# Kernel optimization log

Measured on AMD Instinct MI355X. Metric: run time of the kernel, lower is better.

Reference implementation:

```python
import jax, jax.numpy as jnp
import numpy as np

B, S, D, H, BS = 4, 4096, 1024, 16, 256
DH = D // H  # 64
NB = S // BS  # 16 blocks


def setup_inputs() -> dict:
    key = jax.random.key(0)
    ks = jax.random.split(key, 16)
    sc = 1.0 / np.sqrt(D).astype(np.float32)

    def lin(k):
        return jax.random.normal(k, (D, D), jnp.float32) * sc

    zb = jnp.zeros((D,), jnp.float32)
    return {
        "x": jax.random.normal(ks[0], (B, S, D), jnp.float32),
        "lq_w": lin(ks[1]), "lq_b": zb,
        "lk_w": lin(ks[2]), "lk_b": zb,
        "lv_w": lin(ks[3]), "lv_b": zb,
        "lo_w": lin(ks[4]), "lo_b": zb,
        "pos_bias": jax.random.normal(ks[5], (1, H, BS, BS), jnp.float32) * 0.1,
        "sq_w": lin(ks[6]), "sq_b": zb,
        "sk_w": lin(ks[7]), "sk_b": zb,
        "sv_w": lin(ks[8]), "sv_b": zb,
        "so_w": lin(ks[9]), "so_b": zb,
        "sum_w": lin(ks[10]), "sum_b": zb,
    }


def _mha(x, qw, qb, kw, kb, vw, vb, ow, ob, bias=None):
    # x: [N, L, D] -> multi-head attention, optional additive position bias.
    N, L, _ = x.shape
    q = (x @ qw + qb).reshape(N, L, H, DH).transpose(0, 2, 1, 3)  # [N,H,L,DH]
    k = (x @ kw + kb).reshape(N, L, H, DH).transpose(0, 2, 1, 3)
    v = (x @ vw + vb).reshape(N, L, H, DH).transpose(0, 2, 1, 3)
    scores = jnp.einsum("nhqd,nhkd->nhqk", q, k) / jnp.sqrt(jnp.float32(DH))
    if bias is not None:
        scores = scores + bias[:, :, :L, :L]
    w = jax.nn.softmax(scores, axis=-1)
    ctx = jnp.einsum("nhqk,nhkd->nhqd", w, v)
    ctx = ctx.transpose(0, 2, 1, 3).reshape(N, L, D)
    return ctx @ ow + ob


def reference(x, lq_w, lq_b, lk_w, lk_b, lv_w, lv_b, lo_w, lo_b, pos_bias,
              sq_w, sq_b, sk_w, sk_b, sv_w, sv_b, so_w, so_b, sum_w, sum_b):
    # Local block attention with learned position bias (seq already multiple of BS)
    xb = x.reshape(B * NB, BS, D)
    local = _mha(xb, lq_w, lq_b, lk_w, lk_b, lv_w, lv_b, lo_w, lo_b,
                 bias=pos_bias).reshape(B, S, D)
    # Block summaries: mean-pool each block then linear summarizer
    summaries = x.reshape(B, NB, BS, D).mean(axis=2) @ sum_w + sum_b  # [B,NB,D]
    # Global attention over block summaries (no position bias)
    summ = _mha(summaries, sq_w, sq_b, sk_w, sk_b, sv_w, sv_b, so_w, so_b)
    # Broadcast each block's summary context back to its tokens and combine
    summ_exp = jnp.repeat(summ, BS, axis=1)  # [B,S,D]
    return local + summ_exp
```

## Files before the change

### kernel.cpp

```cpp
#include <hip/hip_runtime.h>
#include <hip/hip_bf16.h>

typedef unsigned short u16;
typedef __bf16 bf16x8 __attribute__((ext_vector_type(8)));
typedef float floatx4 __attribute__((ext_vector_type(4)));
typedef unsigned short u16x4 __attribute__((ext_vector_type(4)));
typedef unsigned short u16x8 __attribute__((ext_vector_type(8)));

__device__ __forceinline__ float b2f(u16 v) {
  unsigned u = ((unsigned)v) << 16;
  return __builtin_bit_cast(float, u);
}
__device__ __forceinline__ u16 f2b(float f) {
  unsigned u = __builtin_bit_cast(unsigned, f);
  unsigned r = (u + 0x7FFFu + ((u >> 16) & 1u)) >> 16;
  return (u16)r;
}
__device__ __forceinline__ void cp16(const u16* g, u16* l) {
  __builtin_amdgcn_global_load_lds(
      (const __attribute__((address_space(1))) unsigned int*)g,
      (__attribute__((address_space(3))) unsigned int*)l, 16, 0, 0);
}

struct GemmArgs {
  const u16* A;
  const u16* BT0; const u16* BT1; const u16* BT2;
  const float* b0; const float* b1; const float* b2;
  const float* summ;
  int srow0;
  u16* C0; u16* C1; u16* C2;
  float* Cf;
};

__global__ __launch_bounds__(256, 2) void gemm_bt(GemmArgs g) {
  const int z = blockIdx.z;
  const u16* A      = g.A;
  const u16* BT     = (z == 0) ? g.BT0 : (z == 1 ? g.BT1 : g.BT2);
  const float* bias = (z == 0) ? g.b0  : (z == 1 ? g.b1  : g.b2);
  u16* C            = (z == 0) ? g.C0  : (z == 1 ? g.C1  : g.C2);

  __shared__ u16 As[128 * 32];
  __shared__ u16 Bs[128 * 32];

  const int tid  = threadIdx.x;
  const int lane = tid & 63;
  const int wave = tid >> 6;
  const int quad = lane >> 4;
  const int cl   = lane & 15;
  const int wm   = wave & 1;
  const int wn   = wave >> 1;

  const size_t row0 = (size_t)blockIdx.x * 128;
  const size_t col0 = (size_t)blockIdx.y * 128;

  const int srow = lane >> 2;
  const int soff = (lane & 3) << 3;

  const u16* gA0 = A + (row0 + (size_t)(wave * 16 + srow)) * 1024 + soff;
  const u16* gA1 = gA0 + (size_t)64 * 1024;
  const u16* gB0 = BT + (col0 + (size_t)(wave * 16 + srow)) * 1024 + soff;
  const u16* gB1 = gB0 + (size_t)64 * 1024;
  u16* lA0 = As + wave * 512 + lane * 8;
  u16* lA1 = lA0 + 2048;
  u16* lB0 = Bs + wave * 512 + lane * 8;
  u16* lB1 = lB0 + 2048;

  floatx4 acc[4][4] = {};

  for (int kt = 0; kt < 1024; kt += 32) {
    __syncthreads();
    cp16(gA0, lA0); cp16(gA1, lA1);
    cp16(gB0, lB0); cp16(gB1, lB1);
    gA0 += 32; gA1 += 32; gB0 += 32; gB1 += 32;
    __syncthreads();
    bf16x8 af[4], bfr[4];
#pragma unroll
    for (int m = 0; m < 4; ++m)
      af[m] = *(const bf16x8*)&As[(wm * 64 + m * 16 + cl) * 32 + quad * 8];
#pragma unroll
    for (int n = 0; n < 4; ++n)
      bfr[n] = *(const bf16x8*)&Bs[(wn * 64 + n * 16 + cl) * 32 + quad * 8];
#pragma unroll
    for (int m = 0; m < 4; ++m)
#pragma unroll
      for (int n = 0; n < 4; ++n)
        acc[m][n] = __builtin_amdgcn_mfma_f32_16x16x32_bf16(af[m], bfr[n],
                                                            acc[m][n], 0, 0, 0);
  }

  const float* summ = g.summ;
#pragma unroll
  for (int m = 0; m < 4; ++m) {
    const size_t rbase = row0 + wm * 64 + m * 16 + quad * 4;
#pragma unroll
    for (int n = 0; n < 4; ++n) {
      const size_t c = col0 + wn * 64 + n * 16 + cl;
      const float bb = bias[c];
#pragma unroll
      for (int e = 0; e < 4; ++e) {
        float v = acc[m][n][e] + bb;
        if (summ)
          v += summ[(size_t)((int)((rbase + e) >> 8) + g.srow0) * 1024 + c];
        if (g.Cf) g.Cf[(rbase + e) * 1024 + c] = v;
        else      C[(rbase + e) * 1024 + c] = f2b(v);
      }
    }
  }
}

__global__ __launch_bounds__(256, 2) void local_attn(
    const u16* __restrict__ Q, const u16* __restrict__ Kt,
    const u16* __restrict__ Vt, const float* __restrict__ pbias,
    u16* __restrict__ ctx) {
  const int qt  = blockIdx.x;
  const int h   = blockIdx.y;
  const int blk = blockIdx.z;
  const int tid  = threadIdx.x;
  const int lane = tid & 63;
  const int w    = tid >> 6;
  const int quad = lane >> 4;
  const int cl   = lane & 15;

  __shared__ u16 BufA[64 * 72];
  __shared__ u16 BufB[64 * 72];

  const size_t tok0  = (size_t)blk * 256;
  const size_t qrow0 = tok0 + qt * 64;
  const int hc = h * 64;

  for (int i = tid; i < 512; i += 256) {
    const int row = i >> 3, c8 = (i & 7) * 8;
    *(u16x8*)&BufA[row * 72 + c8] =
        *(const u16x8*)&Q[(qrow0 + row) * 1024 + hc + c8];
  }

  floatx4 accS[16] = {};
#pragma unroll
  for (int kc = 0; kc < 4; ++kc) {
    __syncthreads();
    for (int i = tid; i < 512; i += 256) {
      const int row = i >> 3, c8 = (i & 7) * 8;
      *(u16x8*)&BufB[row * 72 + c8] =
          *(const u16x8*)&Kt[(tok0 + kc * 64 + row) * 1024 + hc + c8];
    }
    __syncthreads();
#pragma unroll
    for (int ki = 0; ki < 2; ++ki) {
      const bf16x8 aq =
          *(const bf16x8*)&BufA[(w * 16 + cl) * 72 + ki * 32 + quad * 8];
#pragma unroll
      for (int n = 0; n < 4; ++n) {
        const bf16x8 bk =
            *(const bf16x8*)&BufB[(n * 16 + cl) * 72 + ki * 32 + quad * 8];
        accS[kc * 4 + n] = __builtin_amdgcn_mfma_f32_16x16x32_bf16(
            aq, bk, accS[kc * 4 + n], 0, 0, 0);
      }
    }
  }

  float mrow[4] = {-1e30f, -1e30f, -1e30f, -1e30f};
#pragma unroll
  for (int r = 0; r < 4; ++r) {
    const float* brow = pbias + ((size_t)h << 16) +
                        (size_t)(qt * 64 + w * 16 + quad * 4 + r) * 256 + cl;
#pragma unroll
    for (int n = 0; n < 16; ++n) {
      float s = accS[n][r] * 0.125f + brow[n * 16];
      accS[n][r] = s;
      mrow[r] = fmaxf(mrow[r], s);
    }
  }
#pragma unroll
  for (int r = 0; r < 4; ++r) {
#pragma unroll
    for (int st = 1; st < 16; st <<= 1)
      mrow[r] = fmaxf(mrow[r], __shfl_xor(mrow[r], st));
  }
  float lsum[4] = {0.f, 0.f, 0.f, 0.f};
#pragma unroll
  for (int n = 0; n < 16; ++n) {
#pragma unroll
    for (int r = 0; r < 4; ++r) {
      float p = exp2f((accS[n][r] - mrow[r]) * 1.44269504f);
      accS[n][r] = p;
      lsum[r] += p;
    }
  }
#pragma unroll
  for (int r = 0; r < 4; ++r) {
#pragma unroll
    for (int st = 1; st < 16; st <<= 1)
      lsum[r] += __shfl_xor(lsum[r], st);
  }

  floatx4 accO[4] = {};
#pragma unroll
  for (int kc = 0; kc < 4; ++kc) {
    __syncthreads();
#pragma unroll
    for (int nn = 0; nn < 4; ++nn)
#pragma unroll
      for (int r = 0; r < 4; ++r)
        BufA[(w * 16 + quad * 4 + r) * 72 + nn * 16 + cl] =
            f2b(accS[kc * 4 + nn][r]);
    for (int i = tid; i < 512; i += 256) {
      const int key = i & 63, dh0 = (i >> 6) * 8;
      u16x8 v = *(const u16x8*)&Vt[(tok0 + kc * 64 + key) * 1024 + hc + dh0];
#pragma unroll
      for (int j = 0; j < 8; ++j) BufB[(dh0 + j) * 72 + key] = v[j];
    }
    __syncthreads();
#pragma unroll
    for (int ki = 0; ki < 2; ++ki) {
      const bf16x8 ap =
          *(const bf16x8*)&BufA[(w * 16 + cl) * 72 + ki * 32 + quad * 8];
#pragma unroll
      for (int nd = 0; nd < 4; ++nd) {
        const bf16x8 bv =
            *(const bf16x8*)&BufB[(nd * 16 + cl) * 72 + ki * 32 + quad * 8];
        accO[nd] = __builtin_amdgcn_mfma_f32_16x16x32_bf16(ap, bv, accO[nd],
                                                           0, 0, 0);
      }
    }
  }

  float inv[4];
#pragma unroll
  for (int r = 0; r < 4; ++r) inv[r] = 1.0f / lsum[r];
#pragma unroll
  for (int nd = 0; nd < 4; ++nd)
#pragma unroll
    for (int r = 0; r < 4; ++r)
      ctx[(qrow0 + w * 16 + quad * 4 + r) * 1024 + hc + nd * 16 + cl] =
          f2b(accO[nd][r] * inv[r]);
}

__global__ void cvt_x(const float* __restrict__ x, u16* __restrict__ xb) {
  const size_t i = ((size_t)blockIdx.x * 256 + threadIdx.x) * 4;
  float4 v = *(const float4*)&x[i];
  u16x4 o;
  o[0] = f2b(v.x); o[1] = f2b(v.y); o[2] = f2b(v.z); o[3] = f2b(v.w);
  *(u16x4*)&xb[i] = o;
}

__global__ void block_mean(const float* __restrict__ x, u16* __restrict__ xm) {
  const int g = blockIdx.x >> 2;
  const int d = ((blockIdx.x & 3) << 8) + threadIdx.x;
  const float* p = x + (size_t)g * 256 * 1024 + d;
  float s = 0.f;
  for (int t = 0; t < 256; ++t) s += p[(size_t)t * 1024];
  xm[(size_t)g * 1024 + d] = f2b(s * (1.0f / 256.0f));
}

__global__ void summ_attn(const u16* __restrict__ SQ, const u16* __restrict__ SK,
                          const u16* __restrict__ SV, u16* __restrict__ sctx) {
  const int b = blockIdx.x >> 4;
  const int h = blockIdx.x & 15;
  const int t = threadIdx.x;
  __shared__ float Qf[16][64];
  __shared__ float Kf[16][64];
  __shared__ float Vf[16][64];
  __shared__ float sc[16][16];
  for (int i = t; i < 1024; i += 64) {
    const int r = i >> 6, d = i & 63;
    const size_t off = (size_t)(b * 16 + r) * 1024 + h * 64 + d;
    Qf[r][d] = b2f(SQ[off]);
    Kf[r][d] = b2f(SK[off]);
    Vf[r][d] = b2f(SV[off]);
  }
  __syncthreads();
  {
    const int i = t >> 2, j0 = t & 3;
#pragma unroll
    for (int jj = 0; jj < 4; ++jj) {
      const int j = j0 + jj * 4;
      float s = 0.f;
      for (int d = 0; d < 64; ++d) s += Qf[i][d] * Kf[j][d];
      sc[i][j] = s * 0.125f;
    }
  }
  __syncthreads();
  if (t < 16) {
    float m = -1e30f;
    for (int j = 0; j < 16; ++j) m = fmaxf(m, sc[t][j]);
    float l = 0.f;
    for (int j = 0; j < 16; ++j) {
      float p = exp2f((sc[t][j] - m) * 1.44269504f);
      sc[t][j] = p;
      l += p;
    }
    const float inv = 1.0f / l;
    for (int j = 0; j < 16; ++j) sc[t][j] *= inv;
  }
  __syncthreads();
  {
    const int i = t >> 2, d0 = (t & 3) * 16;
    for (int dd = 0; dd < 16; ++dd) {
      float a = 0.f;
      for (int j = 0; j < 16; ++j) a += sc[i][j] * Vf[j][d0 + dd];
      sctx[(size_t)(b * 16 + i) * 1024 + h * 64 + d0 + dd] = f2b(a);
    }
  }
}

struct TPtrs { const float* src[9]; u16* dst[9]; };

__global__ void cvt_transpose9(TPtrs p) {
  const float* src = p.src[blockIdx.z];
  u16* dst         = p.dst[blockIdx.z];
  __shared__ u16 tile[64][72];
  const int r0 = blockIdx.x * 64, c0 = blockIdx.y * 64;
  for (int i = threadIdx.x; i < 1024; i += 256) {
    const int row = i >> 4, c4 = (i & 15) * 4;
    float4 v = *(const float4*)&src[(size_t)(r0 + row) * 1024 + c0 + c4];
    tile[row][c4 + 0] = f2b(v.x);
    tile[row][c4 + 1] = f2b(v.y);
    tile[row][c4 + 2] = f2b(v.z);
    tile[row][c4 + 3] = f2b(v.w);
  }
  __syncthreads();
  for (int i = threadIdx.x; i < 512; i += 256) {
    const int row = i >> 3, c8 = (i & 7) * 8;
    u16x8 v;
#pragma unroll
    for (int j = 0; j < 8; ++j) v[j] = tile[c8 + j][row];
    *(u16x8*)&dst[(size_t)(c0 + row) * 1024 + r0 + c8] = v;
  }
}

extern "C" void kernel_launch(void* const* d_in, const int* in_sizes, int n_in,
                              void* d_out, int out_size, void* d_ws, size_t ws_size,
                              hipStream_t stream) {
  const float* x    = (const float*)d_in[0];
  const float* lqw  = (const float*)d_in[1];
  const float* lqb  = (const float*)d_in[2];
  const float* lkw  = (const float*)d_in[3];
  const float* lkb  = (const float*)d_in[4];
  const float* lvw  = (const float*)d_in[5];
  const float* lvb  = (const float*)d_in[6];
  const float* low_ = (const float*)d_in[7];
  const float* lob  = (const float*)d_in[8];
  const float* pb   = (const float*)d_in[9];
  const float* sqw  = (const float*)d_in[10];
  const float* sqb  = (const float*)d_in[11];
  const float* skw  = (const float*)d_in[12];
  const float* skb  = (const float*)d_in[13];
  const float* svw  = (const float*)d_in[14];
  const float* svb  = (const float*)d_in[15];
  const float* sow  = (const float*)d_in[16];
  const float* sob  = (const float*)d_in[17];
  const float* smw  = (const float*)d_in[18];
  const float* smb  = (const float*)d_in[19];

  char* W = (char*)d_ws;
  size_t off = 0;
  u16* wt[9];
  for (int i = 0; i < 9; ++i) { wt[i] = (u16*)(W + off); off += (size_t)1024 * 1024 * 2; }
  u16* Xb  = (u16*)(W + off); off += (size_t)16384 * 1024 * 2;
  u16* XM  = (u16*)(W + off); off += (size_t)128 * 1024 * 2;
  u16* SMR = (u16*)(W + off); off += (size_t)128 * 1024 * 2;
  u16* SQp = (u16*)(W + off); off += (size_t)128 * 1024 * 2;
  u16* SKp = (u16*)(W + off); off += (size_t)128 * 1024 * 2;
  u16* SVp = (u16*)(W + off); off += (size_t)128 * 1024 * 2;
  u16* SCT = (u16*)(W + off); off += (size_t)128 * 1024 * 2;
  float* SMM = (float*)(W + off); off += (size_t)128 * 1024 * 4;
  const size_t fixedB = off;

  int CH = 256;
  for (int c = 16384; c >= 256; c >>= 1) {
    if (fixedB + (size_t)4 * c * 1024 * 2 <= ws_size) { CH = c; break; }
  }
  u16* Qb  = (u16*)(W + fixedB);
  u16* Kb  = Qb + (size_t)CH * 1024;
  u16* Vb  = Kb + (size_t)CH * 1024;
  u16* CTX = Vb + (size_t)CH * 1024;

  TPtrs tp;
  tp.src[0] = lqw; tp.src[1] = lkw; tp.src[2] = lvw; tp.src[3] = low_;
  tp.src[4] = sqw; tp.src[5] = skw; tp.src[6] = svw; tp.src[7] = sow;
  tp.src[8] = smw;
  for (int i = 0; i < 9; ++i) tp.dst[i] = wt[i];
  cvt_transpose9<<<dim3(16, 16, 9), 256, 0, stream>>>(tp);

  cvt_x<<<dim3(16384), 256, 0, stream>>>(x, Xb);
  block_mean<<<dim3(256), 256, 0, stream>>>(x, XM);

  GemmArgs g1{};
  g1.A = XM; g1.BT0 = g1.BT1 = g1.BT2 = wt[8];
  g1.b0 = g1.b1 = g1.b2 = smb; g1.summ = nullptr; g1.srow0 = 0;
  g1.C0 = g1.C1 = g1.C2 = SMR; g1.Cf = nullptr;
  gemm_bt<<<dim3(1, 8, 1), 256, 0, stream>>>(g1);

  GemmArgs g2{};
  g2.A = SMR; g2.BT0 = wt[4]; g2.BT1 = wt[5]; g2.BT2 = wt[6];
  g2.b0 = sqb; g2.b1 = skb; g2.b2 = svb; g2.summ = nullptr; g2.srow0 = 0;
  g2.C0 = SQp; g2.C1 = SKp; g2.C2 = SVp; g2.Cf = nullptr;
  gemm_bt<<<dim3(1, 8, 3), 256, 0, stream>>>(g2);

  summ_attn<<<dim3(64), 64, 0, stream>>>(SQp, SKp, SVp, SCT);

  GemmArgs g3{};
  g3.A = SCT; g3.BT0 = g3.BT1 = g3.BT2 = wt[7];
  g3.b0 = g3.b1 = g3.b2 = sob; g3.summ = nullptr; g3.srow0 = 0;
  g3.C0 = g3.C1 = g3.C2 = nullptr; g3.Cf = SMM;
  gemm_bt<<<dim3(1, 8, 1), 256, 0, stream>>>(g3);

  for (int base = 0; base < 16384; base += CH) {
    GemmArgs g4{};
    g4.A = Xb + (size_t)base * 1024;
    g4.BT0 = wt[0]; g4.BT1 = wt[1]; g4.BT2 = wt[2];
    g4.b0 = lqb; g4.b1 = lkb; g4.b2 = lvb; g4.summ = nullptr; g4.srow0 = 0;
    g4.C0 = Qb; g4.C1 = Kb; g4.C2 = Vb; g4.Cf = nullptr;
    gemm_bt<<<dim3(CH / 128, 8, 3), 256, 0, stream>>>(g4);

    local_attn<<<dim3(4, 16, CH / 256), 256, 0, stream>>>(Qb, Kb, Vb, pb, CTX);

    GemmArgs g5{};
    g5.A = CTX; g5.BT0 = g5.BT1 = g5.BT2 = wt[3];
    g5.b0 = g5.b1 = g5.b2 = lob; g5.summ = SMM; g5.srow0 = base >> 8;
    g5.C0 = g5.C1 = g5.C2 = nullptr;
    g5.Cf = (float*)d_out + (size_t)base * 1024;
    gemm_bt<<<dim3(CH / 128, 8, 1), 256, 0, stream>>>(g5);
  }

  (void)in_sizes; (void)n_in; (void)out_size;
}
```

Measured before the change: 531.4 us.

## Add 256x256-tile 8-wave GEMM with double-buffered async LDS pipeline

```diff
diff --git a/kernel.cpp b/kernel.cpp
--- a/kernel.cpp
+++ b/kernel.cpp
@@ -92,6 +92,155 @@
 #pragma unroll
   for (int m = 0; m < 4; ++m) {
     const size_t rbase = row0 + wm * 64 + m * 16 + quad * 4;
+#pragma unroll
+    for (int n = 0; n < 4; ++n) {
+      const size_t c = col0 + wn * 64 + n * 16 + cl;
+      const float bb = bias[c];
+#pragma unroll
+      for (int e = 0; e < 4; ++e) {
+        float v = acc[m][n][e] + bb;
+        if (summ)
+          v += summ[(size_t)((int)((rbase + e) >> 8) + g.srow0) * 1024 + c];
+        if (g.Cf) g.Cf[(rbase + e) * 1024 + c] = v;
+        else      C[(rbase + e) * 1024 + c] = f2b(v);
+      }
+    }
+  }
+}
+
+__global__ __launch_bounds__(512, 2) void gemm_bt256(GemmArgs g) {
+  extern __shared__ char lds[];
+  const int z = blockIdx.z;
+  const u16* A      = g.A;
+  const u16* BT     = (z == 0) ? g.BT0 : (z == 1 ? g.BT1 : g.BT2);
+  const float* bias = (z == 0) ? g.b0  : (z == 1 ? g.b1  : g.b2);
+  u16* C            = (z == 0) ? g.C0  : (z == 1 ? g.C1  : g.C2);
+
+  const int tid  = threadIdx.x;
+  const int lane = tid & 63;
+  const int w    = tid >> 6;
+  const int q    = lane >> 4;
+  const int cl   = lane & 15;
+  const int wm   = w >> 2;
+  const int wn   = w & 3;
+
+  const size_t row0 = (size_t)blockIdx.x * 256;
+  const size_t col0 = (size_t)blockIdx.y * 256;
+
+  const int lr  = lane >> 3;
+  const int lcs = ((lane & 7) ^ lr) * 8;
+  const u16* Ab = A  + (row0 + (size_t)lr) * 1024 + lcs;
+  const u16* Bb = BT + (col0 + (size_t)lr) * 1024 + lcs;
+  const int wa8 = w * 8;
+  const int wbr = (w >> 2) * 64 + (w & 3) * 8;
+
+  const int swz  = (cl & 7) << 4;
+  const int aRd0 = (wm * 128 + cl) * 128 + ((q * 16) ^ swz);
+  const int aRd1 = aRd0 ^ 64;
+  const int bRd0 = 32768 + (wn * 64 + cl) * 128 + ((q * 16) ^ swz);
+  const int bRd1 = bRd0 ^ 64;
+
+  floatx4 acc[8][4] = {};
+
+#define STAGE_A(QA, T, BUF)                                                   \
+  {                                                                           \
+    const int r0s = (QA) * 64 + wa8;                                          \
+    cp16(Ab + (size_t)r0s * 1024 + (T) * 64,                                  \
+         (u16*)(lds + (BUF) * 65536 + r0s * 128));                            \
+    const int r1s = r0s + 128;                                                \
+    cp16(Ab + (size_t)r1s * 1024 + (T) * 64,                                  \
+         (u16*)(lds + (BUF) * 65536 + r1s * 128));                            \
+  }
+
+#define STAGE_B(QB, T, BUF)                                                   \
+  {                                                                           \
+    const int r0s = wbr + (QB) * 32;                                          \
+    cp16(Bb + (size_t)r0s * 1024 + (T) * 64,                                  \
+         (u16*)(lds + (BUF) * 65536 + 32768 + r0s * 128));                    \
+    const int r1s = r0s + 128;                                                \
+    cp16(Bb + (size_t)r1s * 1024 + (T) * 64,                                  \
+         (u16*)(lds + (BUF) * 65536 + 32768 + r1s * 128));                    \
+  }
+
+#define PHASE(BUF, QM, QN, STAGE, WAIT)                                       \
+  {                                                                           \
+    char* Lb = lds + (BUF) * 65536;                                           \
+    bf16x8 aF0[4], aF1[4], bF0[2], bF1[2];                                    \
+    _Pragma("unroll")                                                         \
+    for (int mm = 0; mm < 4; ++mm) {                                          \
+      const int ro = ((QM) * 64 + mm * 16) * 128;                             \
+      aF0[mm] = *(const bf16x8*)(Lb + (aRd0 + ro));                           \
+      aF1[mm] = *(const bf16x8*)(Lb + (aRd1 + ro));                           \
+    }                                                                         \
+    _Pragma("unroll")                                                         \
+    for (int nn = 0; nn < 2; ++nn) {                                          \
+      const int co = ((QN) * 32 + nn * 16) * 128;                             \
+      bF0[nn] = *(const bf16x8*)(Lb + (bRd0 + co));                           \
+      bF1[nn] = *(const bf16x8*)(Lb + (bRd1 + co));                           \
+    }                                                                         \
+    STAGE                                                                     \
+    asm volatile("s_barrier" ::: "memory");                                   \
+    asm volatile("s_waitcnt lgkmcnt(0)" ::: "memory");                        \
+    __builtin_amdgcn_s_setprio(1);                                            \
+    _Pragma("unroll")                                                         \
+    for (int mm = 0; mm < 4; ++mm)                                            \
+      _Pragma("unroll")                                                       \
+      for (int nn = 0; nn < 2; ++nn)                                          \
+        acc[(QM) * 4 + mm][(QN) * 2 + nn] =                                   \
+            __builtin_amdgcn_mfma_f32_16x16x32_bf16(                          \
+                aF0[mm], bF0[nn], acc[(QM) * 4 + mm][(QN) * 2 + nn], 0, 0, 0);\
+    _Pragma("unroll")                                                         \
+    for (int mm = 0; mm < 4; ++mm)                                            \
+      _Pragma("unroll")                                                       \
+      for (int nn = 0; nn < 2; ++nn)                                          \
+        acc[(QM) * 4 + mm][(QN) * 2 + nn] =                                   \
+            __builtin_amdgcn_mfma_f32_16x16x32_bf16(                          \
+                aF1[mm], bF1[nn], acc[(QM) * 4 + mm][(QN) * 2 + nn], 0, 0, 0);\
+    __builtin_amdgcn_s_setprio(0);                                            \
+    WAIT                                                                      \
+    asm volatile("s_barrier" ::: "memory");                                   \
+  }
+
+#define TILE_MAIN(BUF, U)                                                     \
+  PHASE(BUF, 0, 0, { STAGE_A(1, (U) + 1, (BUF) ^ 1); }, {})                   \
+  PHASE(BUF, 1, 0, { STAGE_B(1, (U) + 1, (BUF) ^ 1); }, {})                   \
+  PHASE(BUF, 0, 1, { STAGE_B(0, (U) + 2, BUF); }, {})                         \
+  PHASE(BUF, 1, 1, { STAGE_A(0, (U) + 2, BUF); },                             \
+        { asm volatile("s_waitcnt vmcnt(4)" ::: "memory"); })
+
+  STAGE_B(0, 0, 0)
+  STAGE_A(0, 0, 0)
+  STAGE_A(1, 0, 0)
+  STAGE_B(1, 0, 0)
+  STAGE_B(0, 1, 1)
+  STAGE_A(0, 1, 1)
+  asm volatile("s_waitcnt vmcnt(4)" ::: "memory");
+  asm volatile("s_barrier" ::: "memory");
+
+#pragma unroll 1
+  for (int u2 = 0; u2 < 7; ++u2) {
+    const int u0 = u2 * 2;
+    TILE_MAIN(0, u0)
+    TILE_MAIN(1, u0 + 1)
+  }
+  PHASE(0, 0, 0, { STAGE_A(1, 15, 1); }, {})
+  PHASE(0, 1, 0, { STAGE_B(1, 15, 1); }, {})
+  PHASE(0, 0, 1, {}, {})
+  PHASE(0, 1, 1, {}, { asm volatile("s_waitcnt vmcnt(0)" ::: "memory"); })
+  PHASE(1, 0, 0, {}, {})
+  PHASE(1, 1, 0, {}, {})
+  PHASE(1, 0, 1, {}, {})
+  PHASE(1, 1, 1, {}, {})
+
+#undef TILE_MAIN
+#undef PHASE
+#undef STAGE_A
+#undef STAGE_B
+
+  const float* summ = g.summ;
+#pragma unroll
+  for (int m = 0; m < 8; ++m) {
+    const size_t rbase = row0 + wm * 128 + m * 16 + q * 4;
 #pragma unroll
     for (int n = 0; n < 4; ++n) {
       const size_t c = col0 + wn * 64 + n * 16 + cl;
@@ -352,6 +501,14 @@
   const float* smw  = (const float*)d_in[18];
   const float* smb  = (const float*)d_in[19];
 
+  static int s_attr_done = 0;
+  if (!s_attr_done) {
+    (void)hipFuncSetAttribute((const void*)gemm_bt256,
+                              hipFuncAttributeMaxDynamicSharedMemorySize,
+                              131072);
+    s_attr_done = 1;
+  }
+
   char* W = (char*)d_ws;
   size_t off = 0;
   u16* wt[9];
@@ -411,7 +568,7 @@
     g4.BT0 = wt[0]; g4.BT1 = wt[1]; g4.BT2 = wt[2];
     g4.b0 = lqb; g4.b1 = lkb; g4.b2 = lvb; g4.summ = nullptr; g4.srow0 = 0;
     g4.C0 = Qb; g4.C1 = Kb; g4.C2 = Vb; g4.Cf = nullptr;
-    gemm_bt<<<dim3(CH / 128, 8, 3), 256, 0, stream>>>(g4);
+    gemm_bt256<<<dim3(CH / 256, 4, 3), 512, 131072, stream>>>(g4);
 
     local_attn<<<dim3(4, 16, CH / 256), 256, 0, stream>>>(Qb, Kb, Vb, pb, CTX);
 
@@ -420,7 +577,7 @@
     g5.b0 = g5.b1 = g5.b2 = lob; g5.summ = SMM; g5.srow0 = base >> 8;
     g5.C0 = g5.C1 = g5.C2 = nullptr;
     g5.Cf = (float*)d_out + (size_t)base * 1024;
-    gemm_bt<<<dim3(CH / 128, 8, 1), 256, 0, stream>>>(g5);
+    gemm_bt256<<<dim3(CH / 256, 4, 1), 512, 131072, stream>>>(g5);
   }
 
   (void)in_sizes; (void)n_in; (void)out_size;
```

Result: no change. 524.3 us (-1.3%).

## Add 256x256-tile double-buffered GEMM kernel for local QKV and output projections

Applied to the files above, without the earlier changes.

```diff
diff --git a/kernel.cpp b/kernel.cpp
--- a/kernel.cpp
+++ b/kernel.cpp
@@ -92,6 +92,191 @@
 #pragma unroll
   for (int m = 0; m < 4; ++m) {
     const size_t rbase = row0 + wm * 64 + m * 16 + quad * 4;
+#pragma unroll
+    for (int n = 0; n < 4; ++n) {
+      const size_t c = col0 + wn * 64 + n * 16 + cl;
+      const float bb = bias[c];
+#pragma unroll
+      for (int e = 0; e < 4; ++e) {
+        float v = acc[m][n][e] + bb;
+        if (summ)
+          v += summ[(size_t)((int)((rbase + e) >> 8) + g.srow0) * 1024 + c];
+        if (g.Cf) g.Cf[(rbase + e) * 1024 + c] = v;
+        else      C[(rbase + e) * 1024 + c] = f2b(v);
+      }
+    }
+  }
+}
+
+__global__ __launch_bounds__(512, 2) void gemm_bt256(GemmArgs g) {
+  extern __shared__ char lds[];
+  const int z = blockIdx.z;
+  const u16* A      = g.A;
+  const u16* BT     = (z == 0) ? g.BT0 : (z == 1 ? g.BT1 : g.BT2);
+  const float* bias = (z == 0) ? g.b0  : (z == 1 ? g.b1  : g.b2);
+  u16* C            = (z == 0) ? g.C0  : (z == 1 ? g.C1  : g.C2);
+
+  const int tid  = threadIdx.x;
+  const int lane = tid & 63;
+  const int w    = tid >> 6;
+  const int q    = lane >> 4;
+  const int cl   = lane & 15;
+  const int wm   = w >> 2;
+  const int wn   = w & 3;
+
+  const size_t row0 = (size_t)blockIdx.x * 256;
+  const size_t col0 = (size_t)blockIdx.y * 256;
+
+  const int lr  = lane >> 3;
+  const int lcs = ((lane & 7) ^ lr) * 8;
+  const u16* Ab = A  + (row0 + (size_t)lr) * 1024 + lcs;
+  const u16* Bb = BT + (col0 + (size_t)lr) * 1024 + lcs;
+  const int wa8 = w * 8;
+  const int wbr = (w >> 2) * 64 + (w & 3) * 8;
+
+  const int swz = (cl & 7) << 4;
+  const int aB0 = (wm * 128 + cl) * 128 + ((q * 16) ^ swz);
+  const int aB1 = aB0 ^ 64;
+  const int bB0 = 32768 + (wn * 64 + cl) * 128 + ((q * 16) ^ swz);
+  const int bB1 = bB0 ^ 64;
+
+  char* const L0 = lds;
+  char* const L1 = lds + 65536;
+
+  floatx4 acc[8][4] = {};
+  bf16x8 aQ0_0[4], aQ0_1[4], aQ1_0[4], aQ1_1[4];
+  bf16x8 bS0_0[2], bS0_1[2], bS1_0[2], bS1_1[2];
+
+#define VMW(N) asm volatile("s_waitcnt vmcnt(" #N ")" ::: "memory");
+#define LGK0   asm volatile("s_waitcnt lgkmcnt(0)" ::: "memory");
+#define BAR    __builtin_amdgcn_s_barrier();
+
+#define STAGE_A(QA, T, LBASE)                                                 \
+  { const int r0s = (QA) * 64 + wa8;                                          \
+    cp16(Ab + (size_t)r0s * 1024 + (size_t)(T) * 64,                          \
+         (u16*)((LBASE) + r0s * 128));                                        \
+    const int r1s = r0s + 128;                                                \
+    cp16(Ab + (size_t)r1s * 1024 + (size_t)(T) * 64,                          \
+         (u16*)((LBASE) + r1s * 128)); }
+
+#define STAGE_B(QB, T, LBASE)                                                 \
+  { const int r0s = wbr + (QB) * 32;                                          \
+    cp16(Bb + (size_t)r0s * 1024 + (size_t)(T) * 64,                          \
+         (u16*)((LBASE) + 32768 + r0s * 128));                                \
+    const int r1s = r0s + 128;                                                \
+    cp16(Bb + (size_t)r1s * 1024 + (size_t)(T) * 64,                          \
+         (u16*)((LBASE) + 32768 + r1s * 128)); }
+
+#define RD_A(D0, D1, QM, LB)                                                  \
+  _Pragma("unroll") for (int mm = 0; mm < 4; ++mm) {                          \
+    const int ro = (QM) * 8192 + mm * 2048;                                   \
+    D0[mm] = *(const bf16x8*)((LB) + aB0 + ro);                               \
+    D1[mm] = *(const bf16x8*)((LB) + aB1 + ro);                               \
+  }
+
+#define RD_B(D0, D1, QN, LB)                                                  \
+  _Pragma("unroll") for (int nn = 0; nn < 2; ++nn) {                          \
+    const int co = (QN) * 4096 + nn * 2048;                                   \
+    D0[nn] = *(const bf16x8*)((LB) + bB0 + co);                               \
+    D1[nn] = *(const bf16x8*)((LB) + bB1 + co);                               \
+  }
+
+#define MM(QM, QN, A0, A1, B0, B1)                                            \
+  __builtin_amdgcn_s_setprio(1);                                              \
+  _Pragma("unroll") for (int mm = 0; mm < 4; ++mm)                            \
+    _Pragma("unroll") for (int nn = 0; nn < 2; ++nn)                          \
+      acc[(QM) * 4 + mm][(QN) * 2 + nn] =                                     \
+          __builtin_amdgcn_mfma_f32_16x16x32_bf16(                            \
+              A0[mm], B0[nn], acc[(QM) * 4 + mm][(QN) * 2 + nn], 0, 0, 0);    \
+  _Pragma("unroll") for (int mm = 0; mm < 4; ++mm)                            \
+    _Pragma("unroll") for (int nn = 0; nn < 2; ++nn)                          \
+      acc[(QM) * 4 + mm][(QN) * 2 + nn] =                                     \
+          __builtin_amdgcn_mfma_f32_16x16x32_bf16(                            \
+              A1[mm], B1[nn], acc[(QM) * 4 + mm][(QN) * 2 + nn], 0, 0, 0);    \
+  __builtin_amdgcn_s_setprio(0);
+
+  STAGE_A(0, 0, L0) STAGE_B(0, 0, L0) STAGE_B(1, 0, L0) STAGE_A(1, 0, L0)
+  STAGE_A(0, 1, L1) STAGE_B(0, 1, L1) STAGE_B(1, 1, L1) STAGE_A(1, 1, L1)
+  VMW(8)
+  BAR
+  RD_A(aQ0_0, aQ0_1, 0, L0)
+  RD_B(bS0_0, bS0_1, 0, L0)
+  LGK0 BAR
+
+#pragma unroll 1
+  for (int u0 = 0; u0 < 14; u0 += 2) {
+    VMW(8) STAGE_A(0, u0 + 2, L0)
+    RD_B(bS1_0, bS1_1, 1, L0)
+    MM(0, 0, aQ0_0, aQ0_1, bS0_0, bS0_1)
+    LGK0 BAR
+    VMW(8) STAGE_B(0, u0 + 2, L0)
+    RD_A(aQ1_0, aQ1_1, 1, L0)
+    MM(0, 1, aQ0_0, aQ0_1, bS1_0, bS1_1)
+    LGK0 BAR
+    VMW(8) STAGE_B(1, u0 + 2, L0)
+    RD_A(aQ0_0, aQ0_1, 0, L1)
+    MM(1, 1, aQ1_0, aQ1_1, bS1_0, bS1_1)
+    LGK0 BAR
+    VMW(8) STAGE_A(1, u0 + 2, L0)
+    MM(1, 0, aQ1_0, aQ1_1, bS0_0, bS0_1)
+    RD_B(bS0_0, bS0_1, 0, L1)
+    LGK0 BAR
+    VMW(8) STAGE_A(0, u0 + 3, L1)
+    RD_B(bS1_0, bS1_1, 1, L1)
+    MM(0, 0, aQ0_0, aQ0_1, bS0_0, bS0_1)
+    LGK0 BAR
+    VMW(8) STAGE_B(0, u0 + 3, L1)
+    RD_A(aQ1_0, aQ1_1, 1, L1)
+    MM(0, 1, aQ0_0, aQ0_1, bS1_0, bS1_1)
+    LGK0 BAR
+    VMW(8) STAGE_B(1, u0 + 3, L1)
+    RD_A(aQ0_0, aQ0_1, 0, L0)
+    MM(1, 1, aQ1_0, aQ1_1, bS1_0, bS1_1)
+    LGK0 BAR
+    VMW(8) STAGE_A(1, u0 + 3, L1)
+    MM(1, 0, aQ1_0, aQ1_1, bS0_0, bS0_1)
+    RD_B(bS0_0, bS0_1, 0, L0)
+    LGK0 BAR
+  }
+
+  VMW(8)
+  RD_B(bS1_0, bS1_1, 1, L0)
+  MM(0, 0, aQ0_0, aQ0_1, bS0_0, bS0_1)
+  LGK0 BAR
+  VMW(6)
+  RD_A(aQ1_0, aQ1_1, 1, L0)
+  MM(0, 1, aQ0_0, aQ0_1, bS1_0, bS1_1)
+  LGK0 BAR
+  VMW(4)
+  RD_A(aQ0_0, aQ0_1, 0, L1)
+  MM(1, 1, aQ1_0, aQ1_1, bS1_0, bS1_1)
+  LGK0 BAR
+  VMW(2)
+  MM(1, 0, aQ1_0, aQ1_1, bS0_0, bS0_1)
+  RD_B(bS0_0, bS0_1, 0, L1)
+  LGK0 BAR
+  VMW(0)
+  RD_B(bS1_0, bS1_1, 1, L1)
+  MM(0, 0, aQ0_0, aQ0_1, bS0_0, bS0_1)
+  LGK0 BAR
+  RD_A(aQ1_0, aQ1_1, 1, L1)
+  MM(0, 1, aQ0_0, aQ0_1, bS1_0, bS1_1)
+  MM(1, 1, aQ1_0, aQ1_1, bS1_0, bS1_1)
+  MM(1, 0, aQ1_0, aQ1_1, bS0_0, bS0_1)
+
+#undef MM
+#undef RD_B
+#undef RD_A
+#undef STAGE_B
+#undef STAGE_A
+#undef BAR
+#undef LGK0
+#undef VMW
+
+  const float* summ = g.summ;
+#pragma unroll
+  for (int m = 0; m < 8; ++m) {
+    const size_t rbase = row0 + wm * 128 + m * 16 + q * 4;
 #pragma unroll
     for (int n = 0; n < 4; ++n) {
       const size_t c = col0 + wn * 64 + n * 16 + cl;
@@ -352,6 +537,14 @@
   const float* smw  = (const float*)d_in[18];
   const float* smb  = (const float*)d_in[19];
 
+  static int s_attr_done = 0;
+  if (!s_attr_done) {
+    (void)hipFuncSetAttribute((const void*)gemm_bt256,
+                              hipFuncAttributeMaxDynamicSharedMemorySize,
+                              131072);
+    s_attr_done = 1;
+  }
+
   char* W = (char*)d_ws;
   size_t off = 0;
   u16* wt[9];
@@ -411,7 +604,7 @@
     g4.BT0 = wt[0]; g4.BT1 = wt[1]; g4.BT2 = wt[2];
     g4.b0 = lqb; g4.b1 = lkb; g4.b2 = lvb; g4.summ = nullptr; g4.srow0 = 0;
     g4.C0 = Qb; g4.C1 = Kb; g4.C2 = Vb; g4.Cf = nullptr;
-    gemm_bt<<<dim3(CH / 128, 8, 3), 256, 0, stream>>>(g4);
+    gemm_bt256<<<dim3(CH / 256, 4, 3), 512, 131072, stream>>>(g4);
 
     local_attn<<<dim3(4, 16, CH / 256), 256, 0, stream>>>(Qb, Kb, Vb, pb, CTX);
 
@@ -420,7 +613,7 @@
     g5.b0 = g5.b1 = g5.b2 = lob; g5.summ = SMM; g5.srow0 = base >> 8;
     g5.C0 = g5.C1 = g5.C2 = nullptr;
     g5.Cf = (float*)d_out + (size_t)base * 1024;
-    gemm_bt<<<dim3(CH / 128, 8, 1), 256, 0, stream>>>(g5);
+    gemm_bt256<<<dim3(CH / 256, 4, 1), 512, 131072, stream>>>(g5);
   }
 
   (void)in_sizes; (void)n_in; (void)out_size;
```

Result: slower. 658.5 us (+23.9%).

## Add 256x128 double-buffered GEMM kernel with swizzled LDS for big projections

Applied to the files above, without the earlier changes.

```diff
diff --git a/kernel.cpp b/kernel.cpp
--- a/kernel.cpp
+++ b/kernel.cpp
@@ -92,6 +92,156 @@
 #pragma unroll
   for (int m = 0; m < 4; ++m) {
     const size_t rbase = row0 + wm * 64 + m * 16 + quad * 4;
+#pragma unroll
+    for (int n = 0; n < 4; ++n) {
+      const size_t c = col0 + wn * 64 + n * 16 + cl;
+      const float bb = bias[c];
+#pragma unroll
+      for (int e = 0; e < 4; ++e) {
+        float v = acc[m][n][e] + bb;
+        if (summ)
+          v += summ[(size_t)((int)((rbase + e) >> 8) + g.srow0) * 1024 + c];
+        if (g.Cf) g.Cf[(rbase + e) * 1024 + c] = v;
+        else      C[(rbase + e) * 1024 + c] = f2b(v);
+      }
+    }
+  }
+}
+
+__global__ __launch_bounds__(512, 2) void gemm_bt256(GemmArgs g) {
+  extern __shared__ char lds[];
+  const int z = blockIdx.z;
+  const u16* A      = g.A;
+  const u16* BT     = (z == 0) ? g.BT0 : (z == 1 ? g.BT1 : g.BT2);
+  const float* bias = (z == 0) ? g.b0  : (z == 1 ? g.b1  : g.b2);
+  u16* C            = (z == 0) ? g.C0  : (z == 1 ? g.C1  : g.C2);
+
+  const int tid  = threadIdx.x;
+  const int lane = tid & 63;
+  const int w    = tid >> 6;
+  const int q    = lane >> 4;
+  const int cl   = lane & 15;
+  const int wm   = w >> 1;
+  const int wn   = w & 1;
+
+  const size_t row0 = (size_t)blockIdx.x * 256;
+  const size_t col0 = (size_t)blockIdx.y * 128;
+
+  const int lr  = lane >> 3;
+  const int lcs = ((lane & 7) ^ lr) * 8;
+  const u16* Ab = A  + (row0 + (size_t)(lr + w * 8)) * 1024 + lcs;
+  const u16* Bb = BT + (col0 + (size_t)(lr + w * 8)) * 1024 + lcs;
+  const int dOff = w * 1024 + lane * 16;
+
+  const int swz  = (cl & 7) << 4;
+  const int aBs  = (wm * 64 + cl) * 128 + ((q * 16) ^ swz);
+  const int bBs  = 32768 + (wn * 64 + cl) * 128 + ((q * 16) ^ swz);
+
+  char* const L0 = lds;
+  char* const L1 = lds + 49152;
+
+  floatx4 acc[4][4] = {};
+  bf16x8 aA[2][2], aB[2][2], aT[2][2];
+  bf16x8 bA[4][2], bB[4][2];
+
+#define VMW2   asm volatile("s_waitcnt vmcnt(2)" ::: "memory");
+#define VMW0   asm volatile("s_waitcnt vmcnt(0)" ::: "memory");
+#define LGK4   asm volatile("s_waitcnt lgkmcnt(4)" ::: "memory");          \
+               __builtin_amdgcn_sched_barrier(0);
+#define LGK12  asm volatile("s_waitcnt lgkmcnt(12)" ::: "memory");         \
+               __builtin_amdgcn_sched_barrier(0);
+#define LGK0   asm volatile("s_waitcnt lgkmcnt(0)" ::: "memory");          \
+               __builtin_amdgcn_sched_barrier(0);
+#define BAR    __builtin_amdgcn_s_barrier();
+
+#define STAGE_B2(T, LB)                                                       \
+  _Pragma("unroll") for (int j = 0; j < 2; ++j)                               \
+    cp16(Bb + (size_t)(j * 64) * 1024 + (size_t)(T) * 64,                     \
+         (u16*)((LB) + 32768 + j * 8192 + dOff));
+
+#define STAGE_A4(T, LB)                                                       \
+  _Pragma("unroll") for (int j = 0; j < 4; ++j)                               \
+    cp16(Ab + (size_t)(j * 64) * 1024 + (size_t)(T) * 64,                     \
+         (u16*)((LB) + j * 8192 + dOff));
+
+#define RD_AH(D, H, LB)                                                       \
+  _Pragma("unroll") for (int mm = 0; mm < 2; ++mm) {                          \
+    const int a0 = aBs + ((H) * 2 + mm) * 2048;                               \
+    D[mm][0] = *(const bf16x8*)((LB) + a0);                                   \
+    D[mm][1] = *(const bf16x8*)((LB) + (a0 ^ 64));                            \
+  }
+
+#define RD_B8(D, LB)                                                          \
+  _Pragma("unroll") for (int nn = 0; nn < 4; ++nn) {                          \
+    const int b0 = bBs + nn * 2048;                                           \
+    D[nn][0] = *(const bf16x8*)((LB) + b0);                                   \
+    D[nn][1] = *(const bf16x8*)((LB) + (b0 ^ 64));                            \
+  }
+
+#define MM16(MH, AF, BF)                                                      \
+  __builtin_amdgcn_s_setprio(1);                                              \
+  _Pragma("unroll") for (int mm = 0; mm < 2; ++mm)                            \
+    _Pragma("unroll") for (int nn = 0; nn < 4; ++nn) {                        \
+      acc[(MH) * 2 + mm][nn] = __builtin_amdgcn_mfma_f32_16x16x32_bf16(       \
+          AF[mm][0], BF[nn][0], acc[(MH) * 2 + mm][nn], 0, 0, 0);             \
+      acc[(MH) * 2 + mm][nn] = __builtin_amdgcn_mfma_f32_16x16x32_bf16(       \
+          AF[mm][1], BF[nn][1], acc[(MH) * 2 + mm][nn], 0, 0, 0);             \
+    }                                                                         \
+  __builtin_amdgcn_s_setprio(0);
+
+  STAGE_B2(0, L0) STAGE_A4(0, L0)
+  STAGE_B2(1, L1) STAGE_A4(1, L1)
+  VMW0
+  BAR
+  RD_AH(aA, 0, L0) RD_B8(bA, L0)
+  LGK0 BAR
+
+#pragma unroll 1
+  for (int u0 = 0; u0 < 14; u0 += 2) {
+    STAGE_B2(u0 + 2, L0)
+    RD_AH(aT, 1, L0)
+    LGK4  MM16(0, aA, bA)
+    LGK0 VMW2 BAR
+    STAGE_A4(u0 + 2, L0)
+    RD_AH(aB, 0, L1) RD_B8(bB, L1)
+    LGK12 MM16(1, aT, bA)
+    LGK0 BAR
+    STAGE_B2(u0 + 3, L1)
+    RD_AH(aT, 1, L1)
+    LGK4  MM16(0, aB, bB)
+    LGK0 VMW2 BAR
+    STAGE_A4(u0 + 3, L1)
+    RD_AH(aA, 0, L0) RD_B8(bA, L0)
+    LGK12 MM16(1, aT, bB)
+    LGK0 BAR
+  }
+
+  RD_AH(aT, 1, L0)
+  LGK4  MM16(0, aA, bA)
+  LGK0 VMW0 BAR
+  RD_AH(aB, 0, L1) RD_B8(bB, L1)
+  LGK12 MM16(1, aT, bA)
+  LGK0 BAR
+  RD_AH(aT, 1, L1)
+  LGK4  MM16(0, aB, bB)
+  LGK0  MM16(1, aT, bB)
+
+#undef MM16
+#undef RD_B8
+#undef RD_AH
+#undef STAGE_A4
+#undef STAGE_B2
+#undef BAR
+#undef LGK0
+#undef LGK12
+#undef LGK4
+#undef VMW0
+#undef VMW2
+
+  const float* summ = g.summ;
+#pragma unroll
+  for (int m = 0; m < 4; ++m) {
+    const size_t rbase = row0 + wm * 64 + m * 16 + q * 4;
 #pragma unroll
     for (int n = 0; n < 4; ++n) {
       const size_t c = col0 + wn * 64 + n * 16 + cl;
@@ -352,6 +502,14 @@
   const float* smw  = (const float*)d_in[18];
   const float* smb  = (const float*)d_in[19];
 
+  static int s_attr_done = 0;
+  if (!s_attr_done) {
+    (void)hipFuncSetAttribute((const void*)gemm_bt256,
+                              hipFuncAttributeMaxDynamicSharedMemorySize,
+                              98304);
+    s_attr_done = 1;
+  }
+
   char* W = (char*)d_ws;
   size_t off = 0;
   u16* wt[9];
@@ -411,7 +569,7 @@
     g4.BT0 = wt[0]; g4.BT1 = wt[1]; g4.BT2 = wt[2];
     g4.b0 = lqb; g4.b1 = lkb; g4.b2 = lvb; g4.summ = nullptr; g4.srow0 = 0;
     g4.C0 = Qb; g4.C1 = Kb; g4.C2 = Vb; g4.Cf = nullptr;
-    gemm_bt<<<dim3(CH / 128, 8, 3), 256, 0, stream>>>(g4);
+    gemm_bt256<<<dim3(CH / 256, 8, 3), 512, 98304, stream>>>(g4);
 
     local_attn<<<dim3(4, 16, CH / 256), 256, 0, stream>>>(Qb, Kb, Vb, pb, CTX);
 
@@ -420,7 +578,7 @@
     g5.b0 = g5.b1 = g5.b2 = lob; g5.summ = SMM; g5.srow0 = base >> 8;
     g5.C0 = g5.C1 = g5.C2 = nullptr;
     g5.Cf = (float*)d_out + (size_t)base * 1024;
-    gemm_bt<<<dim3(CH / 128, 8, 1), 256, 0, stream>>>(g5);
+    gemm_bt256<<<dim3(CH / 256, 8, 1), 512, 98304, stream>>>(g5);
   }
 
   (void)in_sizes; (void)n_in; (void)out_size;
```

After: 524.6 us. About the same (-1.3%).
